# Performance work log

Measured on AMD Instinct MI355X. Metric: run time of the kernel, lower is better.

Reference implementation:

```python
import jax, jax.numpy as jnp
import numpy as np

J, L, A, A_PRIME, C_CH = 4, 4, 2, 2, 1
B, M, N = 4, 128, 128


def _compute_idx():
    # mirrors CorrLayerDownsample.compute_idx with delta_j=J, delta_l=L,
    # shift_mode='samec' and num_channels=1 (to_shift_color always True)
    dj, dl = J, L
    la1, la2, shifted = [], [], []
    for c1 in range(C_CH):
        for c2 in range(C_CH):
            for j1 in range(J):
                for j2 in range(j1, min(j1 + 1 + dj, J)):
                    for l1 in range(L):
                        for l2 in range(max(0, l1 + 1 - dl), min(L, l1 + 1 + dl)):
                            for a1 in range(A):
                                for a2 in range(A_PRIME):
                                    la1.append((j1, A * L * c1 + A * l1 + a1))
                                    la2.append((j2, A * L * c2 + A * l2 + a2))
                                    shifted.append(j2 + 1)
    return (np.asarray(la1, np.int32), np.asarray(la2, np.int32),
            np.asarray(shifted, np.int32))


def _make_masks():
    # stand-in for create_masks_shift: mask 0 = zero shift only; mask k (k>=1)
    # = wrapped square neighborhood of radius 2**(k-1) (shift scale grows with j2)
    xs = np.minimum(np.arange(M), M - np.arange(M))
    ys = np.minimum(np.arange(N), N - np.arange(N))
    masks = np.zeros((J + 1, M, N), np.float32)
    masks[0, 0, 0] = 1.0
    for k in range(1, J + 1):
        r = 2 ** (k - 1)
        masks[k] = ((xs[:, None] <= r) & (ys[None, :] <= r)).astype(np.float32)
    return masks


def setup_inputs() -> dict:
    key = jax.random.key(0)
    la1, la2, shifted = _compute_idx()
    masks = _make_masks()
    union_idx = np.where(masks.sum(0).reshape(-1) > 0)[0].astype(np.int32)
    xpsi = jax.random.normal(key, (J, B, C_CH * L * A, M, N), dtype=jnp.float32)
    return {
        "xpsi": xpsi,
        "masks_shift": jnp.asarray(masks),
        "la1": jnp.asarray(la1),
        "la2": jnp.asarray(la2),
        "shifted": jnp.asarray(shifted),
        "union_idx": jnp.asarray(union_idx),
    }


def reference(xpsi, masks_shift, la1, la2, shifted, union_idx):
    # xpsi: [J, B, C, M, N] real. FFT once per (scale, channel) map.
    hatx = jnp.fft.fft2(xpsi)                     # [J, B, C, M, N] complex64
    # gather the (scale, la-channel) pair for every moment (all scales same size,
    # so the per-(j1,j2) loop + upsample of the original collapses to one gather)
    h1 = hatx[la1[:, 0], :, la1[:, 1]]            # [P, B, M, N]
    h2 = hatx[la2[:, 0], :, la2[:, 1]]            # [P, B, M, N]
    corr = jnp.fft.ifft2(h1 * jnp.conj(h2)).real  # [P, B, M, N]
    masked = corr * masks_shift[shifted][:, None]  # per-moment shift mask
    P, Bb, Mm, Nn = masked.shape
    # flatten=True path: keep only positions in the union of all shift masks
    return masked.reshape(P, Bb, Mm * Nn)[:, :, union_idx]
```

## Files before the change

kernel.cpp:

```cpp
#include <hip/hip_runtime.h>

typedef __attribute__((ext_vector_type(8))) short short8;
typedef __attribute__((ext_vector_type(4))) float float4v;

#define TPB 256
#define NPART 3207168
#define NOUT  739840

__device__ __constant__ int TBASE[19] = {
    0, 278528, 557056, 835584, 1114112, 1392640, 1671168, 1949696, 2228224,
    2506752, 2617344, 2727936, 2838528, 2949120,
    3059712, 3100672, 3141632,
    3182592, 3194880};
__device__ __constant__ unsigned char J1T[10] = {0,0,0,0,1,1,1,2,2,3};
__device__ __constant__ unsigned char J2T[10] = {0,1,2,3,1,2,3,2,3,3};
__device__ __constant__ unsigned char TSTART[4] = {17,14,9,0};

static __device__ __forceinline__ unsigned short f2bf(float f) {
    unsigned int u = __builtin_bit_cast(unsigned int, f);
    u = (u + 0x7FFFu + ((u >> 16) & 1u)) >> 16;
    return (unsigned short)u;
}

template<int J2, bool PART>
static __device__ __forceinline__ void corr_body(
        const float* __restrict__ xpsi,
        float* __restrict__ out, float* __restrict__ part,
        unsigned char* smem, int tgl, int n0, int moff, int b, int kc)
{
    constexpr int R    = 1 << J2;
    constexpr int DXN  = 2 * R + 1;
    constexpr int DYN  = DXN;
    constexpr int MV   = 8 * (J2 + 1);
    constexpr int ROWS = 16 + 2 * R;
    constexpr int ABUF = 16 * 256;
    constexpr int S    = DYN * MV * 16;
    constexpr int W    = (J2 == 0) ? 8 : 16;

    unsigned short* a_lds = (unsigned short*)smem;
    unsigned short* b_lds = (unsigned short*)(smem + 4 * ABUF);

    const int k0    = kc * 16;
    const int vrows = (MV - moff < 16) ? MV - moff : 16;

    const int ch2lo = n0 / DXN;
    int nhi = n0 + W - 1; if (nhi > 8 * DXN - 1) nhi = 8 * DXN - 1;
    const int nimg = nhi / DXN - ch2lo + 1;

    const int tid  = threadIdx.x;
    const int lane = tid & 63;
    const int wv   = tid >> 6;
    const int c    = lane & 15;
    const int g    = lane >> 4;

    const int ncol    = n0 + c;
    const bool validn = (ncol < 8 * DXN) && (J2 > 0 || c < 8);
    const int ncc     = validn ? ncol : n0;
    const int ch2     = ncc / DXN;
    const int dxi     = ncc - ch2 * DXN;
    const int dx      = dxi - R;
    const int xo      = dx < 0 ? dx + 17 : dx;
    const int bst     = ((ch2 - ch2lo) * ROWS + (2 * R - dxi)) * 152;

    float4 ar[4];
    auto loadA = [&](int sub) {
        #pragma unroll
        for (int it = 0; it < 2; ++it) {
            const int o  = it * TPB + tid;
            const int ms = o >> 5;
            const int lo = (o & 31) ^ ms;
            const int me = moff + ms;
            const int j1 = me >> 3, ch1 = me & 7;
            if (ms < vrows) {
                const float* s = xpsi + ((((size_t)j1*4 + b)*8) + ch1) * 16384
                               + (k0 + sub * 2 + (lo >> 4)) * 128 + ((lo & 15) << 3);
                ar[2*it]   = ((const float4*)s)[0];
                ar[2*it+1] = ((const float4*)s)[1];
            } else {
                ar[2*it]   = float4{0.f,0.f,0.f,0.f};
                ar[2*it+1] = float4{0.f,0.f,0.f,0.f};
            }
        }
    };
    auto writeA = [&](int bufi) {
        unsigned short* ab = a_lds + bufi * ABUF;
        #pragma unroll
        for (int it = 0; it < 2; ++it) {
            const int o = it * TPB + tid;
            const float4 f0 = ar[2*it], f1 = ar[2*it+1];
            *(ushort4*)(ab + o * 8)     = ushort4{f2bf(f0.x),f2bf(f0.y),f2bf(f0.z),f2bf(f0.w)};
            *(ushort4*)(ab + o * 8 + 4) = ushort4{f2bf(f1.x),f2bf(f1.y),f2bf(f1.z),f2bf(f1.w)};
        }
    };

    loadA(0);

    if (J2 >= 2) {
        for (int ci = 0; ci < nimg; ++ci) {
            const float* img = xpsi + ((((size_t)J2*4 + b)*8) + ch2lo + ci) * 16384;
            const int ng2 = ROWS * 36;
            for (int i = tid; i < ng2; i += TPB) {
                const int tr = i / 36, tc = (i - tr * 36) * 4;
                const int sr = (k0 - R + tr) & 127;
                const int sc = (tc + R - 16) & 127;
                const float4 v = *(const float4*)(img + sr * 128 + sc);
                *(ushort4*)(b_lds + (ci * ROWS + tr) * 152 + tc) =
                    ushort4{f2bf(v.x), f2bf(v.y), f2bf(v.z), f2bf(v.w)};
            }
        }
    } else {
        const int tot = nimg * ROWS * 144;
        for (int i = tid; i < tot; i += TPB) {
            const int ci = i / (ROWS * 144);
            const int rr = i - ci * (ROWS * 144);
            const int tr = rr / 144, tc = rr - tr * 144;
            const int sr = (k0 - R + tr) & 127;
            const int sc = (tc + R - 16) & 127;
            b_lds[(ci * ROWS + tr) * 152 + tc] =
                f2bf(xpsi[((((size_t)J2*4 + b)*8) + ch2lo + ci) * 16384 + sr * 128 + sc]);
        }
    }

    writeA(0);

    float4v acc[DYN];
    #pragma unroll
    for (int i = 0; i < DYN; ++i) acc[i] = (float4v)0.f;

    auto compute = [&](int sub, int bufi) {
        const char* abase = (const char*)(a_lds + bufi * ABUF);
        #pragma unroll
        for (int i2 = 0; i2 < 2; ++i2) {
            const int loff = (((i2 << 8) | (wv << 6) | (g << 4))) ^ (c << 4);
            const short8 af0 = *(const short8*)(abase + c * 512 + loff);

            const unsigned short* bp = b_lds + bst + (sub * 2 + i2) * 152
                                     + (wv << 5) + (g << 3);
            const uint4 wA = *(const uint4*)bp;
            const uint4 wB = *(const uint4*)(bp + 8);
            const uint4 wC = *(const uint4*)(bp + 16);
            const unsigned int wd[12] = {wA.x,wA.y,wA.z,wA.w, wB.x,wB.y,wB.z,wB.w,
                                         wC.x,wC.y,wC.z,wC.w};
            #pragma unroll
            for (int dyi = 0; dyi < DYN; ++dyi) {
                unsigned int o0, o1, o2, o3;
                if ((dyi & 1) == 0) {
                    const int bb = 8 - (dyi >> 1);
                    o0 = wd[bb]; o1 = wd[bb+1]; o2 = wd[bb+2]; o3 = wd[bb+3];
                } else {
                    const int bb = (15 - dyi) >> 1;
                    o0 = (wd[bb]   >> 16) | (wd[bb+1] << 16);
                    o1 = (wd[bb+1] >> 16) | (wd[bb+2] << 16);
                    o2 = (wd[bb+2] >> 16) | (wd[bb+3] << 16);
                    o3 = (wd[bb+3] >> 16) | (wd[bb+4] << 16);
                }
                union { unsigned int u[4]; short8 s; } bq;
                bq.u[0] = o0; bq.u[1] = o1; bq.u[2] = o2; bq.u[3] = o3;
                acc[dyi] = __builtin_amdgcn_mfma_f32_16x16x32_bf16(
                    af0, bq.s, acc[dyi], 0, 0, 0);
            }
        }
    };

    __syncthreads();
    for (int sub = 0; sub < 8; ++sub) {
        if (sub < 7) loadA(sub + 1);
        compute(sub, sub & 1);
        if (sub < 7) writeA((sub + 1) & 1);
        __syncthreads();
    }

    if (PART) {
        constexpr int NG  = (DYN < 9) ? DYN : 9;
        constexpr int NPH = (DYN + NG - 1) / NG;
        float* red = (float*)smem;
        float* pt  = part + TBASE[tgl] + (size_t)(kc * 4 + b) * S;
        const int cpart0 = n0 & 15;
        #pragma unroll
        for (int ph = 0; ph < NPH; ++ph) {
            const int d0 = ph * NG;
            const int nd = (DYN - d0 < NG) ? (DYN - d0) : NG;
            __syncthreads();
            #pragma unroll
            for (int dl = 0; dl < NG; ++dl) {
                if (dl >= nd) break;
                *(float4v*)(red + ((wv * NG + dl) * 64 + lane) * 4) = acc[d0 + dl];
            }
            __syncthreads();
            for (int i = tid; i < nd * 64; i += TPB) {
                const int dl = i >> 6;
                const int ln = i & 63;
                const float4v s0 = *(const float4v*)(red + ((0 * NG + dl) * 64 + ln) * 4);
                const float4v s1 = *(const float4v*)(red + ((1 * NG + dl) * 64 + ln) * 4);
                const float4v s2 = *(const float4v*)(red + ((2 * NG + dl) * 64 + ln) * 4);
                const float4v s3 = *(const float4v*)(red + ((3 * NG + dl) * 64 + ln) * 4);
                const float4v s = (s0 + s1) + (s2 + s3);
                const int cc = ln & 15, gg = ln >> 4;
                if ((n0 + cc < 8 * DXN) && (J2 > 0 || cc < 8)) {
                    const int dyi = d0 + dl;
                    #pragma unroll
                    for (int t2 = 0; t2 < 4; ++t2) {
                        const int ml = (gg << 2) + t2;
                        if (ml < vrows)
                            pt[(dyi * MV + moff + ml) * 16 + cpart0 + cc] = s[t2];
                    }
                }
            }
        }
        return;
    }

    if (!validn) return;
    #pragma unroll
    for (int dyi = 0; dyi < DYN; ++dyi) {
        const int dy = dyi - R;
        const int yo = dy < 0 ? dy + 17 : dy;
        #pragma unroll
        for (int t2 = 0; t2 < 4; ++t2) {
            const int ml = (g << 2) + t2;
            if (ml >= vrows) continue;
            const int m = moff + ml;
            const int j1 = m >> 3, ch1 = m & 7;
            const int pb = ((j1 * (9 - j1)) >> 1) + (J2 - j1);
            const int p  = pb * 64 + ((ch1 >> 1) << 4) + ((ch2 >> 1) << 2)
                         + ((ch1 & 1) << 1) + (ch2 & 1);
            atomicAdd(out + (size_t)(p * 4 + b) * 289 + xo * 17 + yo, acc[dyi][t2]);
        }
    }
}

template<bool PART>
__global__ __launch_bounds__(TPB, 3)
void corr_v9(const float* __restrict__ xpsi,
             float* __restrict__ out, float* __restrict__ part)
{
    __shared__ __align__(16) unsigned char smem[40704];
    const int bid = blockIdx.x;
    const int g8  = bid & 7;
    const int b   = g8 >> 1;
    const int mh  = g8 & 1;
    const int w   = bid >> 3;
    const int kc  = w / 17;
    const int s   = w - kc * 17;
    if (s < 9)
        corr_body<3, PART>(xpsi, out, part, smem, s, 16 * s, 16 * mh, b, kc);
    else if (s < 14)
        corr_body<2, PART>(xpsi, out, part, smem, s, 16 * (s - 9), 16 * mh, b, kc);
    else if (mh == 0)
        corr_body<1, PART>(xpsi, out, part, smem, s, 16 * (s - 14), 0, b, kc);
    else
        corr_body<0, PART>(xpsi, out, part, smem,
                           (s < 16) ? 17 : 18, 8 * (s - 14), 0, b, kc);
}

__global__ __launch_bounds__(256)
void reduce_k(const float* __restrict__ part, float* __restrict__ out)
{
    const int o = blockIdx.x * 256 + threadIdx.x;
    if (o >= NOUT) return;
    const int p  = o / 1156;
    const int r1 = o - p * 1156;
    const int b  = r1 / 289;
    const int s  = r1 - b * 289;
    const int xo = s / 17, yo = s - xo * 17;
    const int pb = p >> 6, cc = p & 63;
    const int j1 = J1T[pb], j2 = J2T[pb];
    const int R  = 1 << j2;
    const int dx = xo <= 8 ? xo : xo - 17;
    const int dy = yo <= 8 ? yo : yo - 17;
    float v = 0.f;
    if (dx >= -R && dx <= R && dy >= -R && dy <= R) {
        const int ch1 = ((cc >> 4) & 3) * 2 + ((cc >> 1) & 1);
        const int ch2 = ((cc >> 2) & 3) * 2 + (cc & 1);
        const int DYN = 2 * R + 1, MV = 8 * (j2 + 1);
        const int ncol = ch2 * DYN + (dx + R);
        const int t = TSTART[j2] + (ncol >> 4);
        const int c = ncol & 15;
        const int m = j1 * 8 + ch1;
        const int S = DYN * MV * 16;
        const float* q = part + TBASE[t]
                       + ((size_t)(b * DYN + (dy + R)) * MV + m) * 16 + c;
        #pragma unroll
        for (int kc = 0; kc < 8; ++kc) v += q[(size_t)kc * 4 * S];
    }
    out[o] = v;
}

extern "C" void kernel_launch(void* const* d_in, const int* in_sizes, int n_in,
                              void* d_out, int out_size, void* d_ws, size_t ws_size,
                              hipStream_t stream) {
    const float* xpsi = (const float*)d_in[0];
    float* out = (float*)d_out;

    if (ws_size >= (size_t)NPART * 4) {
        float* part = (float*)d_ws;
        corr_v9<true><<<1088, TPB, 0, stream>>>(xpsi, out, part);
        reduce_k<<<(NOUT + 255) / 256, 256, 0, stream>>>(part, out);
    } else {
        hipMemsetAsync(d_out, 0, (size_t)out_size * sizeof(float), stream);
        corr_v9<false><<<1088, TPB, 0, stream>>>(xpsi, out, nullptr);
    }
}
```

Measured before the change: 45.35 us.

## Pre-convert input to bf16 and stage A tiles via direct global-to-LDS loads

Measured after the change: 54.96 us. 1.21x slower.

```diff
diff --git a/kernel.cpp b/kernel.cpp
--- a/kernel.cpp
+++ b/kernel.cpp
@@ -2,10 +2,17 @@
 
 typedef __attribute__((ext_vector_type(8))) short short8;
 typedef __attribute__((ext_vector_type(4))) float float4v;
+typedef __attribute__((address_space(1))) const unsigned int gu32;
+typedef __attribute__((address_space(3))) unsigned int lu32;
 
 #define TPB 256
+#define NXPSI (4*4*8*16384)
+#define NGR   (NXPSI/4)
+#define ZPG   64
+#define PBYTE (NXPSI*2 + ZPG*8)
 #define NPART 3207168
 #define NOUT  739840
+#define NENT  21
 
 __device__ __constant__ int TBASE[19] = {
     0, 278528, 557056, 835584, 1114112, 1392640, 1671168, 1949696, 2228224,
@@ -16,15 +23,34 @@
 __device__ __constant__ unsigned char J2T[10] = {0,1,2,3,1,2,3,2,3,3};
 __device__ __constant__ unsigned char TSTART[4] = {17,14,9,0};
 
+__device__ __constant__ unsigned char E_N0[NENT] = {
+    0,32,64,96,128, 0,32,64,96,128, 0,32,64, 0,32,64, 0,16,32, 0,16};
+__device__ __constant__ unsigned char E_MOFF[NENT] = {
+    0,0,0,0,0, 16,16,16,16,16, 0,0,0, 16,16,16, 0,0,0, 0,0};
+__device__ __constant__ unsigned char E_TG[NENT] = {
+    0,2,4,6,8, 0,2,4,6,8, 9,11,13, 9,11,13, 14,15,16, 17,18};
+
 static __device__ __forceinline__ unsigned short f2bf(float f) {
     unsigned int u = __builtin_bit_cast(unsigned int, f);
     u = (u + 0x7FFFu + ((u >> 16) & 1u)) >> 16;
     return (unsigned short)u;
 }
 
-template<int J2, bool PART>
+__global__ __launch_bounds__(256)
+void conv_bf16(const float* __restrict__ in, unsigned short* __restrict__ outw) {
+    const int g = blockIdx.x * 256 + threadIdx.x;
+    if (g < NGR) {
+        const float4 v = reinterpret_cast<const float4*>(in)[g];
+        reinterpret_cast<ushort4*>(outw)[g] =
+            ushort4{f2bf(v.x), f2bf(v.y), f2bf(v.z), f2bf(v.w)};
+    } else if (g < NGR + ZPG) {
+        reinterpret_cast<ushort4*>(outw)[g] = ushort4{0, 0, 0, 0};
+    }
+}
+
+template<int J2, bool PRE, bool PART>
 static __device__ __forceinline__ void corr_body(
-        const float* __restrict__ xpsi,
+        const float* __restrict__ xpsi, const unsigned short* __restrict__ xbf,
         float* __restrict__ out, float* __restrict__ part,
         unsigned char* smem, int tgl, int n0, int moff, int b, int kc)
 {
@@ -35,7 +61,8 @@
     constexpr int ROWS = 16 + 2 * R;
     constexpr int ABUF = 16 * 256;
     constexpr int S    = DYN * MV * 16;
-    constexpr int W    = (J2 == 0) ? 8 : 16;
+    constexpr int W    = (J2 >= 2) ? 32 : 16;
+    constexpr int F    = W / 16;
 
     unsigned short* a_lds = (unsigned short*)smem;
     unsigned short* b_lds = (unsigned short*)(smem + 4 * ABUF);
@@ -53,16 +80,38 @@
     const int c    = lane & 15;
     const int g    = lane >> 4;
 
-    const int ncol    = n0 + c;
-    const bool validn = (ncol < 8 * DXN) && (J2 > 0 || c < 8);
-    const int ncc     = validn ? ncol : n0;
-    const int ch2     = ncc / DXN;
-    const int dxi     = ncc - ch2 * DXN;
-    const int dx      = dxi - R;
-    const int xo      = dx < 0 ? dx + 17 : dx;
-    const int bst     = ((ch2 - ch2lo) * ROWS + (2 * R - dxi)) * 152;
+    const int ncolA  = n0 + c;
+    const bool validA = ncolA < 8 * DXN;
+    const int nccA   = validA ? ncolA : (8 * DXN - 1);
+    const int ch2A   = nccA / DXN;
+    const int dxiA   = nccA - ch2A * DXN;
+    const int bstA   = ((ch2A - ch2lo) * ROWS + (2 * R - dxiA)) * 152;
+    const int ncolB  = n0 + 16 + c;
+    const bool validB = (W == 32) && (ncolB < 8 * DXN);
+    const int nccB   = (ncolB < 8 * DXN) ? ncolB : (8 * DXN - 1);
+    const int ch2B   = nccB / DXN;
+    const int dxiB   = nccB - ch2B * DXN;
+    const int bstB   = ((ch2B - ch2lo) * ROWS + (2 * R - dxiB)) * 152;
 
     float4 ar[4];
+    auto stageA = [&](int sub, int bufi) {
+        unsigned short* ab = a_lds + bufi * ABUF;
+        #pragma unroll
+        for (int it = 0; it < 2; ++it) {
+            const int o  = it * TPB + tid;
+            const int ms = o >> 5;
+            const int lo = (o & 31) ^ ms;
+            const int me = moff + ms;
+            const int j1 = me >> 3, ch1 = me & 7;
+            if (PRE) {
+                const unsigned short* src = (ms < vrows)
+                    ? xbf + ((((size_t)j1*4 + b)*8) + ch1) * 16384
+                          + (k0 + sub * 2 + (lo >> 4)) * 128 + ((lo & 15) << 3)
+                    : xbf + NXPSI + ((lo & 31) << 3);
+                __builtin_amdgcn_global_load_lds((gu32*)src, (lu32*)(ab + o * 8), 16, 0, 0);
+            }
+        }
+    };
     auto loadA = [&](int sub) {
         #pragma unroll
         for (int it = 0; it < 2; ++it) {
@@ -77,8 +126,7 @@
                 ar[2*it]   = ((const float4*)s)[0];
                 ar[2*it+1] = ((const float4*)s)[1];
             } else {
-                ar[2*it]   = float4{0.f,0.f,0.f,0.f};
-                ar[2*it+1] = float4{0.f,0.f,0.f,0.f};
+                ar[2*it] = float4{0,0,0,0}; ar[2*it+1] = float4{0,0,0,0};
             }
         }
     };
@@ -88,24 +136,23 @@
         for (int it = 0; it < 2; ++it) {
             const int o = it * TPB + tid;
             const float4 f0 = ar[2*it], f1 = ar[2*it+1];
-            *(ushort4*)(ab + o * 8)     = ushort4{f2bf(f0.x),f2bf(f0.y),f2bf(f0.z),f2bf(f0.w)};
-            *(ushort4*)(ab + o * 8 + 4) = ushort4{f2bf(f1.x),f2bf(f1.y),f2bf(f1.z),f2bf(f1.w)};
+            *(ushort4*)(ab + o*8)   = ushort4{f2bf(f0.x),f2bf(f0.y),f2bf(f0.z),f2bf(f0.w)};
+            *(ushort4*)(ab + o*8+4) = ushort4{f2bf(f1.x),f2bf(f1.y),f2bf(f1.z),f2bf(f1.w)};
         }
     };
 
-    loadA(0);
-
-    if (J2 >= 2) {
+    if (PRE) stageA(0, 0); else loadA(0);
+
+    if (PRE && J2 >= 2) {
         for (int ci = 0; ci < nimg; ++ci) {
-            const float* img = xpsi + ((((size_t)J2*4 + b)*8) + ch2lo + ci) * 16384;
+            const unsigned short* img = xbf + ((((size_t)J2*4 + b)*8) + ch2lo + ci) * 16384;
             const int ng2 = ROWS * 36;
             for (int i = tid; i < ng2; i += TPB) {
                 const int tr = i / 36, tc = (i - tr * 36) * 4;
                 const int sr = (k0 - R + tr) & 127;
                 const int sc = (tc + R - 16) & 127;
-                const float4 v = *(const float4*)(img + sr * 128 + sc);
                 *(ushort4*)(b_lds + (ci * ROWS + tr) * 152 + tc) =
-                    ushort4{f2bf(v.x), f2bf(v.y), f2bf(v.z), f2bf(v.w)};
+                    *(const ushort4*)(img + sr * 128 + sc);
             }
         }
     } else {
@@ -116,16 +163,20 @@
             const int tr = rr / 144, tc = rr - tr * 144;
             const int sr = (k0 - R + tr) & 127;
             const int sc = (tc + R - 16) & 127;
-            b_lds[(ci * ROWS + tr) * 152 + tc] =
-                f2bf(xpsi[((((size_t)J2*4 + b)*8) + ch2lo + ci) * 16384 + sr * 128 + sc]);
-        }
-    }
-
-    writeA(0);
-
-    float4v acc[DYN];
+            const size_t off = ((((size_t)J2*4 + b)*8) + ch2lo + ci) * 16384 + sr * 128 + sc;
+            b_lds[(ci * ROWS + tr) * 152 + tc] = PRE ? xbf[off] : f2bf(xpsi[off]);
+        }
+    }
+
+    if (!PRE) writeA(0);
+
+    float4v accA[DYN], accB[(W == 32) ? DYN : 1];
     #pragma unroll
-    for (int i = 0; i < DYN; ++i) acc[i] = (float4v)0.f;
+    for (int i = 0; i < DYN; ++i) accA[i] = (float4v)0.f;
+    if (W == 32) {
+        #pragma unroll
+        for (int i = 0; i < DYN; ++i) accB[i] = (float4v)0.f;
+    }
 
     auto compute = [&](int sub, int bufi) {
         const char* abase = (const char*)(a_lds + bufi * ABUF);
@@ -133,124 +184,153 @@
         for (int i2 = 0; i2 < 2; ++i2) {
             const int loff = (((i2 << 8) | (wv << 6) | (g << 4))) ^ (c << 4);
             const short8 af0 = *(const short8*)(abase + c * 512 + loff);
-
-            const unsigned short* bp = b_lds + bst + (sub * 2 + i2) * 152
-                                     + (wv << 5) + (g << 3);
-            const uint4 wA = *(const uint4*)bp;
-            const uint4 wB = *(const uint4*)(bp + 8);
-            const uint4 wC = *(const uint4*)(bp + 16);
-            const unsigned int wd[12] = {wA.x,wA.y,wA.z,wA.w, wB.x,wB.y,wB.z,wB.w,
-                                         wC.x,wC.y,wC.z,wC.w};
-            #pragma unroll
-            for (int dyi = 0; dyi < DYN; ++dyi) {
-                unsigned int o0, o1, o2, o3;
-                if ((dyi & 1) == 0) {
-                    const int bb = 8 - (dyi >> 1);
-                    o0 = wd[bb]; o1 = wd[bb+1]; o2 = wd[bb+2]; o3 = wd[bb+3];
-                } else {
-                    const int bb = (15 - dyi) >> 1;
-                    o0 = (wd[bb]   >> 16) | (wd[bb+1] << 16);
-                    o1 = (wd[bb+1] >> 16) | (wd[bb+2] << 16);
-                    o2 = (wd[bb+2] >> 16) | (wd[bb+3] << 16);
-                    o3 = (wd[bb+3] >> 16) | (wd[bb+4] << 16);
+            {
+                const unsigned short* bp = b_lds + bstA + (sub*2 + i2)*152 + (wv<<5) + (g<<3);
+                const uint4 wA = *(const uint4*)bp;
+                const uint4 wB = *(const uint4*)(bp + 8);
+                const uint4 wC = *(const uint4*)(bp + 16);
+                const unsigned int wd[12] = {wA.x,wA.y,wA.z,wA.w, wB.x,wB.y,wB.z,wB.w,
+                                             wC.x,wC.y,wC.z,wC.w};
+                #pragma unroll
+                for (int dyi = 0; dyi < DYN; ++dyi) {
+                    unsigned int o0,o1,o2,o3;
+                    if ((dyi & 1) == 0) {
+                        const int bb = 8 - (dyi >> 1);
+                        o0=wd[bb]; o1=wd[bb+1]; o2=wd[bb+2]; o3=wd[bb+3];
+                    } else {
+                        const int bb = (15 - dyi) >> 1;
+                        o0=(wd[bb]>>16)|(wd[bb+1]<<16);   o1=(wd[bb+1]>>16)|(wd[bb+2]<<16);
+                        o2=(wd[bb+2]>>16)|(wd[bb+3]<<16); o3=(wd[bb+3]>>16)|(wd[bb+4]<<16);
+                    }
+                    union { unsigned int u[4]; short8 s; } bq;
+                    bq.u[0]=o0; bq.u[1]=o1; bq.u[2]=o2; bq.u[3]=o3;
+                    accA[dyi] = __builtin_amdgcn_mfma_f32_16x16x32_bf16(
+                        af0, bq.s, accA[dyi], 0, 0, 0);
                 }
-                union { unsigned int u[4]; short8 s; } bq;
-                bq.u[0] = o0; bq.u[1] = o1; bq.u[2] = o2; bq.u[3] = o3;
-                acc[dyi] = __builtin_amdgcn_mfma_f32_16x16x32_bf16(
-                    af0, bq.s, acc[dyi], 0, 0, 0);
+            }
+            if (W == 32) {
+                const unsigned short* bp = b_lds + bstB + (sub*2 + i2)*152 + (wv<<5) + (g<<3);
+                const uint4 wA = *(const uint4*)bp;
+                const uint4 wB = *(const uint4*)(bp + 8);
+                const uint4 wC = *(const uint4*)(bp + 16);
+                const unsigned int wd[12] = {wA.x,wA.y,wA.z,wA.w, wB.x,wB.y,wB.z,wB.w,
+                                             wC.x,wC.y,wC.z,wC.w};
+                #pragma unroll
+                for (int dyi = 0; dyi < DYN; ++dyi) {
+                    unsigned int o0,o1,o2,o3;
+                    if ((dyi & 1) == 0) {
+                        const int bb = 8 - (dyi >> 1);
+                        o0=wd[bb]; o1=wd[bb+1]; o2=wd[bb+2]; o3=wd[bb+3];
+                    } else {
+                        const int bb = (15 - dyi) >> 1;
+                        o0=(wd[bb]>>16)|(wd[bb+1]<<16);   o1=(wd[bb+1]>>16)|(wd[bb+2]<<16);
+                        o2=(wd[bb+2]>>16)|(wd[bb+3]<<16); o3=(wd[bb+3]>>16)|(wd[bb+4]<<16);
+                    }
+                    union { unsigned int u[4]; short8 s; } bq;
+                    bq.u[0]=o0; bq.u[1]=o1; bq.u[2]=o2; bq.u[3]=o3;
+                    accB[dyi] = __builtin_amdgcn_mfma_f32_16x16x32_bf16(
+                        af0, bq.s, accB[dyi], 0, 0, 0);
+                }
             }
         }
     };
 
     __syncthreads();
     for (int sub = 0; sub < 8; ++sub) {
-        if (sub < 7) loadA(sub + 1);
+        if (sub < 7) { if (PRE) stageA(sub + 1, (sub + 1) & 1); else loadA(sub + 1); }
         compute(sub, sub & 1);
-        if (sub < 7) writeA((sub + 1) & 1);
+        if (!PRE && sub < 7) writeA((sub + 1) & 1);
         __syncthreads();
     }
 
     if (PART) {
-        constexpr int NG  = (DYN < 9) ? DYN : 9;
-        constexpr int NPH = (DYN + NG - 1) / NG;
-        float* red = (float*)smem;
-        float* pt  = part + TBASE[tgl] + (size_t)(kc * 4 + b) * S;
-        const int cpart0 = n0 & 15;
-        #pragma unroll
-        for (int ph = 0; ph < NPH; ++ph) {
-            const int d0 = ph * NG;
-            const int nd = (DYN - d0 < NG) ? (DYN - d0) : NG;
-            __syncthreads();
+        auto reduce_store = [&](auto& accv, int tg, int nb) {
+            constexpr int NG  = (DYN < 9) ? DYN : 9;
+            constexpr int NPH = (DYN + NG - 1) / NG;
+            float* red = (float*)smem;
+            float* pt  = part + TBASE[tg] + (size_t)(kc * 4 + b) * S;
             #pragma unroll
-            for (int dl = 0; dl < NG; ++dl) {
-                if (dl >= nd) break;
-                *(float4v*)(red + ((wv * NG + dl) * 64 + lane) * 4) = acc[d0 + dl];
-            }
-            __syncthreads();
-            for (int i = tid; i < nd * 64; i += TPB) {
-                const int dl = i >> 6;
-                const int ln = i & 63;
-                const float4v s0 = *(const float4v*)(red + ((0 * NG + dl) * 64 + ln) * 4);
-                const float4v s1 = *(const float4v*)(red + ((1 * NG + dl) * 64 + ln) * 4);
-                const float4v s2 = *(const float4v*)(red + ((2 * NG + dl) * 64 + ln) * 4);
-                const float4v s3 = *(const float4v*)(red + ((3 * NG + dl) * 64 + ln) * 4);
-                const float4v s = (s0 + s1) + (s2 + s3);
-                const int cc = ln & 15, gg = ln >> 4;
-                if ((n0 + cc < 8 * DXN) && (J2 > 0 || cc < 8)) {
-                    const int dyi = d0 + dl;
-                    #pragma unroll
-                    for (int t2 = 0; t2 < 4; ++t2) {
-                        const int ml = (gg << 2) + t2;
-                        if (ml < vrows)
-                            pt[(dyi * MV + moff + ml) * 16 + cpart0 + cc] = s[t2];
+            for (int ph = 0; ph < NPH; ++ph) {
+                const int d0 = ph * NG;
+                const int nd = (DYN - d0 < NG) ? (DYN - d0) : NG;
+                __syncthreads();
+                #pragma unroll
+                for (int dl = 0; dl < NG; ++dl) {
+                    if (dl >= nd) break;
+                    *(float4v*)(red + ((wv * NG + dl) * 64 + lane) * 4) = accv[d0 + dl];
+                }
+                __syncthreads();
+                for (int i = tid; i < nd * 64; i += TPB) {
+                    const int dl = i >> 6, ln = i & 63;
+                    const float4v s0 = *(const float4v*)(red + ((0*NG + dl)*64 + ln)*4);
+                    const float4v s1 = *(const float4v*)(red + ((1*NG + dl)*64 + ln)*4);
+                    const float4v s2 = *(const float4v*)(red + ((2*NG + dl)*64 + ln)*4);
+                    const float4v s3 = *(const float4v*)(red + ((3*NG + dl)*64 + ln)*4);
+                    const float4v s = (s0 + s1) + (s2 + s3);
+                    const int cc = ln & 15, gg = ln >> 4;
+                    if (nb + cc < 8 * DXN) {
+                        const int dyi = d0 + dl;
+                        #pragma unroll
+                        for (int t2 = 0; t2 < 4; ++t2) {
+                            const int ml = (gg << 2) + t2;
+                            if (ml < vrows)
+                                pt[(dyi * MV + moff + ml) * 16 + cc] = s[t2];
+                        }
                     }
                 }
             }
-        }
+        };
+        reduce_store(accA, tgl, n0);
+        if (W == 32 && n0 + 16 < 8 * DXN)
+            reduce_store(accB, tgl + 1, n0 + 16);
         return;
     }
 
-    if (!validn) return;
     #pragma unroll
-    for (int dyi = 0; dyi < DYN; ++dyi) {
-        const int dy = dyi - R;
-        const int yo = dy < 0 ? dy + 17 : dy;
-        #pragma unroll
-        for (int t2 = 0; t2 < 4; ++t2) {
-            const int ml = (g << 2) + t2;
-            if (ml >= vrows) continue;
-            const int m = moff + ml;
-            const int j1 = m >> 3, ch1 = m & 7;
-            const int pb = ((j1 * (9 - j1)) >> 1) + (J2 - j1);
-            const int p  = pb * 64 + ((ch1 >> 1) << 4) + ((ch2 >> 1) << 2)
-                         + ((ch1 & 1) << 1) + (ch2 & 1);
-            atomicAdd(out + (size_t)(p * 4 + b) * 289 + xo * 17 + yo, acc[dyi][t2]);
-        }
-    }
-}
-
-template<bool PART>
-__global__ __launch_bounds__(TPB, 3)
-void corr_v9(const float* __restrict__ xpsi,
-             float* __restrict__ out, float* __restrict__ part)
+    for (int f = 0; f < F; ++f) {
+        const bool vf = f ? validB : validA;
+        if (!vf) continue;
+        const int ch2 = f ? ch2B : ch2A;
+        const int dx  = (f ? dxiB : dxiA) - R;
+        const int xo  = dx < 0 ? dx + 17 : dx;
+        #pragma unroll
+        for (int dyi = 0; dyi < DYN; ++dyi) {
+            const int dy = dyi - R;
+            const int yo = dy < 0 ? dy + 17 : dy;
+            #pragma unroll
+            for (int t2 = 0; t2 < 4; ++t2) {
+                const int ml = (g << 2) + t2;
+                if (ml >= vrows) continue;
+                const int m = moff + ml;
+                const int j1 = m >> 3, ch1 = m & 7;
+                const int pb = ((j1 * (9 - j1)) >> 1) + (J2 - j1);
+                const int p  = pb * 64 + ((ch1 >> 1) << 4) + ((ch2 >> 1) << 2)
+                             + ((ch1 & 1) << 1) + (ch2 & 1);
+                const float val = f ? accB[dyi][t2] : accA[dyi][t2];
+                atomicAdd(out + (size_t)(p * 4 + b) * 289 + xo * 17 + yo, val);
+            }
+        }
+    }
+}
+
+template<bool PRE, bool PART>
+__global__ __launch_bounds__(TPB, 2)
+void corr_v10(const float* __restrict__ xpsi, const unsigned short* __restrict__ xbf,
+              float* __restrict__ out, float* __restrict__ part)
 {
-    __shared__ __align__(16) unsigned char smem[40704];
+    __shared__ __align__(16) unsigned char smem[52864];
     const int bid = blockIdx.x;
-    const int g8  = bid & 7;
-    const int b   = g8 >> 1;
-    const int mh  = g8 & 1;
-    const int w   = bid >> 3;
-    const int kc  = w / 17;
-    const int s   = w - kc * 17;
-    if (s < 9)
-        corr_body<3, PART>(xpsi, out, part, smem, s, 16 * s, 16 * mh, b, kc);
-    else if (s < 14)
-        corr_body<2, PART>(xpsi, out, part, smem, s, 16 * (s - 9), 16 * mh, b, kc);
-    else if (mh == 0)
-        corr_body<1, PART>(xpsi, out, part, smem, s, 16 * (s - 14), 0, b, kc);
-    else
-        corr_body<0, PART>(xpsi, out, part, smem,
-                           (s < 16) ? 17 : 18, 8 * (s - 14), 0, b, kc);
+    const int e   = bid >> 5;
+    const int rem = bid & 31;
+    const int b   = rem & 3;
+    const int kc  = rem >> 2;
+    const int n0   = E_N0[e];
+    const int moff = E_MOFF[e];
+    const int tgl  = E_TG[e];
+    if (e < 10)      corr_body<3, PRE, PART>(xpsi, xbf, out, part, smem, tgl, n0, moff, b, kc);
+    else if (e < 16) corr_body<2, PRE, PART>(xpsi, xbf, out, part, smem, tgl, n0, moff, b, kc);
+    else if (e < 19) corr_body<1, PRE, PART>(xpsi, xbf, out, part, smem, tgl, n0, moff, b, kc);
+    else             corr_body<0, PRE, PART>(xpsi, xbf, out, part, smem, tgl, n0, moff, b, kc);
 }
 
 __global__ __launch_bounds__(256)
@@ -292,12 +372,19 @@
     const float* xpsi = (const float*)d_in[0];
     float* out = (float*)d_out;
 
-    if (ws_size >= (size_t)NPART * 4) {
-        float* part = (float*)d_ws;
-        corr_v9<true><<<1088, TPB, 0, stream>>>(xpsi, out, part);
+    if (ws_size >= (size_t)PBYTE + (size_t)NPART * 4) {
+        unsigned short* xbf = (unsigned short*)d_ws;
+        float* part = (float*)((char*)d_ws + PBYTE);
+        conv_bf16<<<(NGR + ZPG + 255) / 256, 256, 0, stream>>>(xpsi, xbf);
+        corr_v10<true, true><<<NENT * 32, TPB, 0, stream>>>(xpsi, xbf, out, part);
         reduce_k<<<(NOUT + 255) / 256, 256, 0, stream>>>(part, out);
+    } else if (ws_size >= (size_t)PBYTE) {
+        unsigned short* xbf = (unsigned short*)d_ws;
+        hipMemsetAsync(d_out, 0, (size_t)out_size * sizeof(float), stream);
+        conv_bf16<<<(NGR + ZPG + 255) / 256, 256, 0, stream>>>(xpsi, xbf);
+        corr_v10<true, false><<<NENT * 32, TPB, 0, stream>>>(xpsi, xbf, out, nullptr);
     } else {
         hipMemsetAsync(d_out, 0, (size_t)out_size * sizeof(float), stream);
-        corr_v9<false><<<1088, TPB, 0, stream>>>(xpsi, out, nullptr);
-    }
-}
+        corr_v10<false, false><<<NENT * 32, TPB, 0, stream>>>(xpsi, nullptr, out, nullptr);
+    }
+}
```

## Split waves across k-halves and dy groups to halve accumulators per wave

Applied to the files above, without the earlier changes.

New measurement: 76.71 us. 69.1% more time.

```diff
diff --git a/kernel.cpp b/kernel.cpp
--- a/kernel.cpp
+++ b/kernel.cpp
@@ -31,6 +31,8 @@
     constexpr int R    = 1 << J2;
     constexpr int DXN  = 2 * R + 1;
     constexpr int DYN  = DXN;
+    constexpr int NH   = (DYN + 1) / 2;
+    constexpr int ND2  = DYN - NH;
     constexpr int MV   = 8 * (J2 + 1);
     constexpr int ROWS = 16 + 2 * R;
     constexpr int ABUF = 16 * 256;
@@ -50,6 +52,8 @@
     const int tid  = threadIdx.x;
     const int lane = tid & 63;
     const int wv   = tid >> 6;
+    const int kh   = wv & 1;
+    const int dg   = wv >> 1;
     const int c    = lane & 15;
     const int g    = lane >> 4;
 
@@ -77,8 +81,7 @@
                 ar[2*it]   = ((const float4*)s)[0];
                 ar[2*it+1] = ((const float4*)s)[1];
             } else {
-                ar[2*it]   = float4{0.f,0.f,0.f,0.f};
-                ar[2*it+1] = float4{0.f,0.f,0.f,0.f};
+                ar[2*it] = float4{0.f,0.f,0.f,0.f}; ar[2*it+1] = float4{0.f,0.f,0.f,0.f};
             }
         }
     };
@@ -88,8 +91,8 @@
         for (int it = 0; it < 2; ++it) {
             const int o = it * TPB + tid;
             const float4 f0 = ar[2*it], f1 = ar[2*it+1];
-            *(ushort4*)(ab + o * 8)     = ushort4{f2bf(f0.x),f2bf(f0.y),f2bf(f0.z),f2bf(f0.w)};
-            *(ushort4*)(ab + o * 8 + 4) = ushort4{f2bf(f1.x),f2bf(f1.y),f2bf(f1.z),f2bf(f1.w)};
+            *(ushort4*)(ab + o*8)   = ushort4{f2bf(f0.x),f2bf(f0.y),f2bf(f0.z),f2bf(f0.w)};
+            *(ushort4*)(ab + o*8+4) = ushort4{f2bf(f1.x),f2bf(f1.y),f2bf(f1.z),f2bf(f1.w)};
         }
     };
 
@@ -123,41 +126,60 @@
 
     writeA(0);
 
-    float4v acc[DYN];
+    float4v acc[NH];
     #pragma unroll
-    for (int i = 0; i < DYN; ++i) acc[i] = (float4v)0.f;
+    for (int i = 0; i < NH; ++i) acc[i] = (float4v)0.f;
 
     auto compute = [&](int sub, int bufi) {
         const char* abase = (const char*)(a_lds + bufi * ABUF);
         #pragma unroll
-        for (int i2 = 0; i2 < 2; ++i2) {
-            const int loff = (((i2 << 8) | (wv << 6) | (g << 4))) ^ (c << 4);
+        for (int i2 = 0; i2 < 4; ++i2) {
+            const int loff = (((kh << 8) | (i2 << 6) | (g << 4))) ^ (c << 4);
             const short8 af0 = *(const short8*)(abase + c * 512 + loff);
 
-            const unsigned short* bp = b_lds + bst + (sub * 2 + i2) * 152
-                                     + (wv << 5) + (g << 3);
+            const unsigned short* bp = b_lds + bst + (sub*2 + kh)*152 + (i2<<5) + (g<<3);
             const uint4 wA = *(const uint4*)bp;
             const uint4 wB = *(const uint4*)(bp + 8);
             const uint4 wC = *(const uint4*)(bp + 16);
             const unsigned int wd[12] = {wA.x,wA.y,wA.z,wA.w, wB.x,wB.y,wB.z,wB.w,
                                          wC.x,wC.y,wC.z,wC.w};
-            #pragma unroll
-            for (int dyi = 0; dyi < DYN; ++dyi) {
-                unsigned int o0, o1, o2, o3;
-                if ((dyi & 1) == 0) {
-                    const int bb = 8 - (dyi >> 1);
-                    o0 = wd[bb]; o1 = wd[bb+1]; o2 = wd[bb+2]; o3 = wd[bb+3];
-                } else {
-                    const int bb = (15 - dyi) >> 1;
-                    o0 = (wd[bb]   >> 16) | (wd[bb+1] << 16);
-                    o1 = (wd[bb+1] >> 16) | (wd[bb+2] << 16);
-                    o2 = (wd[bb+2] >> 16) | (wd[bb+3] << 16);
-                    o3 = (wd[bb+3] >> 16) | (wd[bb+4] << 16);
+            if (dg == 0) {
+                #pragma unroll
+                for (int dyl = 0; dyl < NH; ++dyl) {
+                    constexpr int base = 0;
+                    const int dyi = base + dyl;
+                    unsigned int o0,o1,o2,o3;
+                    if ((dyi & 1) == 0) {
+                        const int bb = 8 - (dyi >> 1);
+                        o0=wd[bb]; o1=wd[bb+1]; o2=wd[bb+2]; o3=wd[bb+3];
+                    } else {
+                        const int bb = (15 - dyi) >> 1;
+                        o0=(wd[bb]>>16)|(wd[bb+1]<<16);   o1=(wd[bb+1]>>16)|(wd[bb+2]<<16);
+                        o2=(wd[bb+2]>>16)|(wd[bb+3]<<16); o3=(wd[bb+3]>>16)|(wd[bb+4]<<16);
+                    }
+                    union { unsigned int u[4]; short8 s; } bq;
+                    bq.u[0]=o0; bq.u[1]=o1; bq.u[2]=o2; bq.u[3]=o3;
+                    acc[dyl] = __builtin_amdgcn_mfma_f32_16x16x32_bf16(
+                        af0, bq.s, acc[dyl], 0, 0, 0);
                 }
-                union { unsigned int u[4]; short8 s; } bq;
-                bq.u[0] = o0; bq.u[1] = o1; bq.u[2] = o2; bq.u[3] = o3;
-                acc[dyi] = __builtin_amdgcn_mfma_f32_16x16x32_bf16(
-                    af0, bq.s, acc[dyi], 0, 0, 0);
+            } else {
+                #pragma unroll
+                for (int dyl = 0; dyl < ND2; ++dyl) {
+                    const int dyi = NH + dyl;
+                    unsigned int o0,o1,o2,o3;
+                    if ((dyi & 1) == 0) {
+                        const int bb = 8 - (dyi >> 1);
+                        o0=wd[bb]; o1=wd[bb+1]; o2=wd[bb+2]; o3=wd[bb+3];
+                    } else {
+                        const int bb = (15 - dyi) >> 1;
+                        o0=(wd[bb]>>16)|(wd[bb+1]<<16);   o1=(wd[bb+1]>>16)|(wd[bb+2]<<16);
+                        o2=(wd[bb+2]>>16)|(wd[bb+3]<<16); o3=(wd[bb+3]>>16)|(wd[bb+4]<<16);
+                    }
+                    union { unsigned int u[4]; short8 s; } bq;
+                    bq.u[0]=o0; bq.u[1]=o1; bq.u[2]=o2; bq.u[3]=o3;
+                    acc[dyl] = __builtin_amdgcn_mfma_f32_16x16x32_bf16(
+                        af0, bq.s, acc[dyl], 0, 0, 0);
+                }
             }
         }
     };
@@ -170,39 +192,34 @@
         __syncthreads();
     }
 
+    const int nmine = dg ? ND2 : NH;
+    const int dy0   = dg ? NH : 0;
+
     if (PART) {
-        constexpr int NG  = (DYN < 9) ? DYN : 9;
-        constexpr int NPH = (DYN + NG - 1) / NG;
         float* red = (float*)smem;
         float* pt  = part + TBASE[tgl] + (size_t)(kc * 4 + b) * S;
         const int cpart0 = n0 & 15;
-        #pragma unroll
-        for (int ph = 0; ph < NPH; ++ph) {
-            const int d0 = ph * NG;
-            const int nd = (DYN - d0 < NG) ? (DYN - d0) : NG;
-            __syncthreads();
+        if (kh == 1) {
             #pragma unroll
-            for (int dl = 0; dl < NG; ++dl) {
-                if (dl >= nd) break;
-                *(float4v*)(red + ((wv * NG + dl) * 64 + lane) * 4) = acc[d0 + dl];
-            }
-            __syncthreads();
-            for (int i = tid; i < nd * 64; i += TPB) {
-                const int dl = i >> 6;
-                const int ln = i & 63;
-                const float4v s0 = *(const float4v*)(red + ((0 * NG + dl) * 64 + ln) * 4);
-                const float4v s1 = *(const float4v*)(red + ((1 * NG + dl) * 64 + ln) * 4);
-                const float4v s2 = *(const float4v*)(red + ((2 * NG + dl) * 64 + ln) * 4);
-                const float4v s3 = *(const float4v*)(red + ((3 * NG + dl) * 64 + ln) * 4);
-                const float4v s = (s0 + s1) + (s2 + s3);
-                const int cc = ln & 15, gg = ln >> 4;
-                if ((n0 + cc < 8 * DXN) && (J2 > 0 || cc < 8)) {
-                    const int dyi = d0 + dl;
+            for (int dyl = 0; dyl < NH; ++dyl) {
+                if (dyl >= nmine) break;
+                *(float4v*)(red + ((dg * NH + dyl) * 64 + lane) * 4) = acc[dyl];
+            }
+        }
+        __syncthreads();
+        if (kh == 0) {
+            #pragma unroll
+            for (int dyl = 0; dyl < NH; ++dyl) {
+                if (dyl >= nmine) break;
+                const float4v s = acc[dyl]
+                    + *(const float4v*)(red + ((dg * NH + dyl) * 64 + lane) * 4);
+                if (validn) {
+                    const int dyi = dy0 + dyl;
                     #pragma unroll
                     for (int t2 = 0; t2 < 4; ++t2) {
-                        const int ml = (gg << 2) + t2;
+                        const int ml = (g << 2) + t2;
                         if (ml < vrows)
-                            pt[(dyi * MV + moff + ml) * 16 + cpart0 + cc] = s[t2];
+                            pt[(dyi * MV + moff + ml) * 16 + cpart0 + c] = s[t2];
                     }
                 }
             }
@@ -212,7 +229,9 @@
 
     if (!validn) return;
     #pragma unroll
-    for (int dyi = 0; dyi < DYN; ++dyi) {
+    for (int dyl = 0; dyl < NH; ++dyl) {
+        if (dyl >= nmine) break;
+        const int dyi = dy0 + dyl;
         const int dy = dyi - R;
         const int yo = dy < 0 ? dy + 17 : dy;
         #pragma unroll
@@ -224,17 +243,17 @@
             const int pb = ((j1 * (9 - j1)) >> 1) + (J2 - j1);
             const int p  = pb * 64 + ((ch1 >> 1) << 4) + ((ch2 >> 1) << 2)
                          + ((ch1 & 1) << 1) + (ch2 & 1);
-            atomicAdd(out + (size_t)(p * 4 + b) * 289 + xo * 17 + yo, acc[dyi][t2]);
+            atomicAdd(out + (size_t)(p * 4 + b) * 289 + xo * 17 + yo, acc[dyl][t2]);
         }
     }
 }
 
 template<bool PART>
-__global__ __launch_bounds__(TPB, 3)
-void corr_v9(const float* __restrict__ xpsi,
-             float* __restrict__ out, float* __restrict__ part)
+__global__ __launch_bounds__(TPB, 4)
+void corr_v11(const float* __restrict__ xpsi,
+              float* __restrict__ out, float* __restrict__ part)
 {
-    __shared__ __align__(16) unsigned char smem[40704];
+    __shared__ __align__(16) unsigned char smem[38272];
     const int bid = blockIdx.x;
     const int g8  = bid & 7;
     const int b   = g8 >> 1;
@@ -294,10 +313,10 @@
 
     if (ws_size >= (size_t)NPART * 4) {
         float* part = (float*)d_ws;
-        corr_v9<true><<<1088, TPB, 0, stream>>>(xpsi, out, part);
+        corr_v11<true><<<1088, TPB, 0, stream>>>(xpsi, out, part);
         reduce_k<<<(NOUT + 255) / 256, 256, 0, stream>>>(part, out);
     } else {
         hipMemsetAsync(d_out, 0, (size_t)out_size * sizeof(float), stream);
-        corr_v9<false><<<1088, TPB, 0, stream>>>(xpsi, out, nullptr);
-    }
-}
+        corr_v11<false><<<1088, TPB, 0, stream>>>(xpsi, out, nullptr);
+    }
+}
```

## Double K-chunk per block, halve grid and partial-sum workspace

Applied to the files above, without the earlier changes.

Result: faster. 43.75 us (median of 3 runs) (-3.5%).

```diff
diff --git a/kernel.cpp b/kernel.cpp
--- a/kernel.cpp
+++ b/kernel.cpp
@@ -4,14 +4,14 @@
 typedef __attribute__((ext_vector_type(4))) float float4v;
 
 #define TPB 256
-#define NPART 3207168
+#define NPART 1603584
 #define NOUT  739840
 
 __device__ __constant__ int TBASE[19] = {
-    0, 278528, 557056, 835584, 1114112, 1392640, 1671168, 1949696, 2228224,
-    2506752, 2617344, 2727936, 2838528, 2949120,
-    3059712, 3100672, 3141632,
-    3182592, 3194880};
+    0, 139264, 278528, 417792, 557056, 696320, 835584, 974848, 1114112,
+    1253376, 1308672, 1363968, 1419264, 1474560,
+    1529856, 1550336, 1570816,
+    1591296, 1597440};
 __device__ __constant__ unsigned char J1T[10] = {0,0,0,0,1,1,1,2,2,3};
 __device__ __constant__ unsigned char J2T[10] = {0,1,2,3,1,2,3,2,3,3};
 __device__ __constant__ unsigned char TSTART[4] = {17,14,9,0};
@@ -40,7 +40,7 @@
     unsigned short* a_lds = (unsigned short*)smem;
     unsigned short* b_lds = (unsigned short*)(smem + 4 * ABUF);
 
-    const int k0    = kc * 16;
+    const int k0    = kc * 32;
     const int vrows = (MV - moff < 16) ? MV - moff : 16;
 
     const int ch2lo = n0 / DXN;
@@ -77,8 +77,7 @@
                 ar[2*it]   = ((const float4*)s)[0];
                 ar[2*it+1] = ((const float4*)s)[1];
             } else {
-                ar[2*it]   = float4{0.f,0.f,0.f,0.f};
-                ar[2*it+1] = float4{0.f,0.f,0.f,0.f};
+                ar[2*it] = float4{0.f,0.f,0.f,0.f}; ar[2*it+1] = float4{0.f,0.f,0.f,0.f};
             }
         }
     };
@@ -88,54 +87,55 @@
         for (int it = 0; it < 2; ++it) {
             const int o = it * TPB + tid;
             const float4 f0 = ar[2*it], f1 = ar[2*it+1];
-            *(ushort4*)(ab + o * 8)     = ushort4{f2bf(f0.x),f2bf(f0.y),f2bf(f0.z),f2bf(f0.w)};
-            *(ushort4*)(ab + o * 8 + 4) = ushort4{f2bf(f1.x),f2bf(f1.y),f2bf(f1.z),f2bf(f1.w)};
+            *(ushort4*)(ab + o*8)   = ushort4{f2bf(f0.x),f2bf(f0.y),f2bf(f0.z),f2bf(f0.w)};
+            *(ushort4*)(ab + o*8+4) = ushort4{f2bf(f1.x),f2bf(f1.y),f2bf(f1.z),f2bf(f1.w)};
         }
     };
 
+    auto stageB = [&](int h) {
+        if (J2 >= 2) {
+            for (int ci = 0; ci < nimg; ++ci) {
+                const float* img = xpsi + ((((size_t)J2*4 + b)*8) + ch2lo + ci) * 16384;
+                const int ng2 = ROWS * 36;
+                for (int i = tid; i < ng2; i += TPB) {
+                    const int tr = i / 36, tc = (i - tr * 36) * 4;
+                    const int sr = (k0 + h * 16 - R + tr) & 127;
+                    const int sc = (tc + R - 16) & 127;
+                    const float4 v = *(const float4*)(img + sr * 128 + sc);
+                    *(ushort4*)(b_lds + (ci * ROWS + tr) * 152 + tc) =
+                        ushort4{f2bf(v.x), f2bf(v.y), f2bf(v.z), f2bf(v.w)};
+                }
+            }
+        } else {
+            const int tot = nimg * ROWS * 144;
+            for (int i = tid; i < tot; i += TPB) {
+                const int ci = i / (ROWS * 144);
+                const int rr = i - ci * (ROWS * 144);
+                const int tr = rr / 144, tc = rr - tr * 144;
+                const int sr = (k0 + h * 16 - R + tr) & 127;
+                const int sc = (tc + R - 16) & 127;
+                b_lds[(ci * ROWS + tr) * 152 + tc] =
+                    f2bf(xpsi[((((size_t)J2*4 + b)*8) + ch2lo + ci) * 16384 + sr * 128 + sc]);
+            }
+        }
+    };
+
     loadA(0);
-
-    if (J2 >= 2) {
-        for (int ci = 0; ci < nimg; ++ci) {
-            const float* img = xpsi + ((((size_t)J2*4 + b)*8) + ch2lo + ci) * 16384;
-            const int ng2 = ROWS * 36;
-            for (int i = tid; i < ng2; i += TPB) {
-                const int tr = i / 36, tc = (i - tr * 36) * 4;
-                const int sr = (k0 - R + tr) & 127;
-                const int sc = (tc + R - 16) & 127;
-                const float4 v = *(const float4*)(img + sr * 128 + sc);
-                *(ushort4*)(b_lds + (ci * ROWS + tr) * 152 + tc) =
-                    ushort4{f2bf(v.x), f2bf(v.y), f2bf(v.z), f2bf(v.w)};
-            }
-        }
-    } else {
-        const int tot = nimg * ROWS * 144;
-        for (int i = tid; i < tot; i += TPB) {
-            const int ci = i / (ROWS * 144);
-            const int rr = i - ci * (ROWS * 144);
-            const int tr = rr / 144, tc = rr - tr * 144;
-            const int sr = (k0 - R + tr) & 127;
-            const int sc = (tc + R - 16) & 127;
-            b_lds[(ci * ROWS + tr) * 152 + tc] =
-                f2bf(xpsi[((((size_t)J2*4 + b)*8) + ch2lo + ci) * 16384 + sr * 128 + sc]);
-        }
-    }
-
+    stageB(0);
     writeA(0);
 
     float4v acc[DYN];
     #pragma unroll
     for (int i = 0; i < DYN; ++i) acc[i] = (float4v)0.f;
 
-    auto compute = [&](int sub, int bufi) {
+    auto compute = [&](int s8, int bufi) {
         const char* abase = (const char*)(a_lds + bufi * ABUF);
         #pragma unroll
         for (int i2 = 0; i2 < 2; ++i2) {
             const int loff = (((i2 << 8) | (wv << 6) | (g << 4))) ^ (c << 4);
             const short8 af0 = *(const short8*)(abase + c * 512 + loff);
 
-            const unsigned short* bp = b_lds + bst + (sub * 2 + i2) * 152
-                                     + (wv << 5) + (g << 3);
+            const unsigned short* bp = b_lds + bst + (s8*2 + i2)*152 + (wv<<5) + (g<<3);
             const uint4 wA = *(const uint4*)bp;
             const uint4 wB = *(const uint4*)(bp + 8);
             const uint4 wC = *(const uint4*)(bp + 16);
@@ -143,19 +143,17 @@
                                          wC.x,wC.y,wC.z,wC.w};
             #pragma unroll
             for (int dyi = 0; dyi < DYN; ++dyi) {
-                unsigned int o0, o1, o2, o3;
+                unsigned int o0,o1,o2,o3;
                 if ((dyi & 1) == 0) {
                     const int bb = 8 - (dyi >> 1);
-                    o0 = wd[bb]; o1 = wd[bb+1]; o2 = wd[bb+2]; o3 = wd[bb+3];
+                    o0=wd[bb]; o1=wd[bb+1]; o2=wd[bb+2]; o3=wd[bb+3];
                 } else {
                     const int bb = (15 - dyi) >> 1;
-                    o0 = (wd[bb]   >> 16) | (wd[bb+1] << 16);
-                    o1 = (wd[bb+1] >> 16) | (wd[bb+2] << 16);
-                    o2 = (wd[bb+2] >> 16) | (wd[bb+3] << 16);
-                    o3 = (wd[bb+3] >> 16) | (wd[bb+4] << 16);
+                    o0=(wd[bb]>>16)|(wd[bb+1]<<16);   o1=(wd[bb+1]>>16)|(wd[bb+2]<<16);
+                    o2=(wd[bb+2]>>16)|(wd[bb+3]<<16); o3=(wd[bb+3]>>16)|(wd[bb+4]<<16);
                 }
                 union { unsigned int u[4]; short8 s; } bq;
-                bq.u[0] = o0; bq.u[1] = o1; bq.u[2] = o2; bq.u[3] = o3;
+                bq.u[0]=o0; bq.u[1]=o1; bq.u[2]=o2; bq.u[3]=o3;
                 acc[dyi] = __builtin_amdgcn_mfma_f32_16x16x32_bf16(
                     af0, bq.s, acc[dyi], 0, 0, 0);
             }
@@ -163,11 +161,18 @@
     };
 
     __syncthreads();
-    for (int sub = 0; sub < 8; ++sub) {
-        if (sub < 7) loadA(sub + 1);
-        compute(sub, sub & 1);
-        if (sub < 7) writeA((sub + 1) & 1);
-        __syncthreads();
+    for (int h = 0; h < 2; ++h) {
+        for (int s8 = 0; s8 < 8; ++s8) {
+            const int sub = h * 8 + s8;
+            if (sub < 15) loadA(sub + 1);
+            compute(s8, sub & 1);
+            if (sub < 15) writeA((sub + 1) & 1);
+            __syncthreads();
+        }
+        if (h == 0) {
+            stageB(1);
+            __syncthreads();
+        }
     }
 
     if (PART) {
@@ -231,10 +236,10 @@
 
 template<bool PART>
 __global__ __launch_bounds__(TPB, 3)
-void corr_v9(const float* __restrict__ xpsi,
-             float* __restrict__ out, float* __restrict__ part)
+void corr_v13(const float* __restrict__ xpsi,
+              float* __restrict__ out, float* __restrict__ part)
 {
-    __shared__ __align__(16) unsigned char smem[40704];
+    __shared__ __align__(16) unsigned char smem[38272];
     const int bid = blockIdx.x;
     const int g8  = bid & 7;
     const int b   = g8 >> 1;
@@ -281,7 +286,7 @@
         const float* q = part + TBASE[t]
                        + ((size_t)(b * DYN + (dy + R)) * MV + m) * 16 + c;
         #pragma unroll
-        for (int kc = 0; kc < 8; ++kc) v += q[(size_t)kc * 4 * S];
+        for (int kc = 0; kc < 4; ++kc) v += q[(size_t)kc * 4 * S];
     }
     out[o] = v;
 }
@@ -294,10 +299,10 @@
 
     if (ws_size >= (size_t)NPART * 4) {
         float* part = (float*)d_ws;
-        corr_v9<true><<<1088, TPB, 0, stream>>>(xpsi, out, part);
+        corr_v13<true><<<544, TPB, 0, stream>>>(xpsi, out, part);
         reduce_k<<<(NOUT + 255) / 256, 256, 0, stream>>>(part, out);
     } else {
         hipMemsetAsync(d_out, 0, (size_t)out_size * sizeof(float), stream);
-        corr_v9<false><<<1088, TPB, 0, stream>>>(xpsi, out, nullptr);
-    }
-}
+        corr_v13<false><<<544, TPB, 0, stream>>>(xpsi, out, nullptr);
+    }
+}
```
